# Kernel optimization log

Hardware: AMD Instinct MI355X
Metric: run time of the kernel (lower is better)

The kernel has to match this reference:

```python
import jax, jax.numpy as jnp
import numpy as np

NEG_INF = -1e9  # same masked_fill constant as the torch module
ALPHA = 0.1     # LeakyReLU negative slope


def setup_inputs() -> dict:
    key = jax.random.key(0)
    k1, k2, k3, k4, k5 = jax.random.split(key, 5)
    B, N, Din, Dout = 8, 2048, 512, 512
    features = jax.random.normal(k1, (B, N, Din), dtype=jnp.float32)
    graph = jax.random.randint(k2, (B, N, N), 0, 2, dtype=jnp.int64)
    # xavier_uniform with gain=1.414: limit = gain*sqrt(6/(fan_in+fan_out))
    lim_w = 1.414 * np.sqrt(6.0 / (Din + Dout))
    w = jax.random.uniform(k3, (Din, Dout), jnp.float32, -lim_w, lim_w)
    lim_a = 1.414 * np.sqrt(6.0 / (Dout + 1))
    a1 = jax.random.uniform(k4, (Dout, 1), jnp.float32, -lim_a, lim_a)
    a2 = jax.random.uniform(k5, (Dout, 1), jnp.float32, -lim_a, lim_a)
    return {"features": features, "graph": graph, "w": w, "a1": a1, "a2": a2}


def reference(features, graph, w, a1, a2):
    # hidden: [B, N, Dout]
    hidden = jnp.einsum("bni,io->bno", features, w)
    s1 = hidden @ a1  # [B, N, 1] -> broadcasts over columns
    s2 = hidden @ a2  # [B, N, 1] -> transposed broadcasts over rows
    # e[b,i,j] = leaky_relu(s1[b,i] + s2[b,j])
    e = jax.nn.leaky_relu(s1 + jnp.swapaxes(s2, 1, 2), negative_slope=ALPHA)
    e = jnp.where(graph == 0, NEG_INF, e)
    attn = jax.nn.softmax(e, axis=-1)  # [B, N, N]; dropout p=0 -> identity
    h_prime = jnp.einsum("bij,bjo->bio", attn, hidden)
    return jax.nn.elu(h_prime)  # concat=True
```

## Files before the change

kernel.cpp:

```cpp
#include <hip/hip_runtime.h>
#include <math.h>

#define B_ 8
#define N_ 2048
#define D_ 512
#define NROWS (B_ * N_)
#define HTS (NROWS + 32)
#define NEG_ALPHA 0.1f

typedef __bf16 bf16;
typedef __bf16 bf16x4 __attribute__((ext_vector_type(4)));
typedef __bf16 bf16x8 __attribute__((ext_vector_type(8)));
typedef float f32x4 __attribute__((ext_vector_type(4)));
typedef float f32x16 __attribute__((ext_vector_type(16)));

__global__ __launch_bounds__(256) void k_prep_wa(const float* __restrict__ W,
                                                 const float* __restrict__ a1,
                                                 const float* __restrict__ a2,
                                                 bf16* __restrict__ Wt,
                                                 float* __restrict__ wa1,
                                                 float* __restrict__ wa2) {
  const int t = threadIdx.x;
  const int bid = blockIdx.x;
#pragma unroll
  for (int p = 0; p < 2; ++p) {
    int din = t + p * 256;
    Wt[bid * D_ + din] = (bf16)W[(size_t)din * D_ + bid];
  }
  if (bid < 128) {
    const int wv = t >> 6, lane = t & 63;
    const int row = bid * 4 + wv;
    const float* wr = W + (size_t)row * D_;
    float d1 = 0.f, d2 = 0.f;
#pragma unroll
    for (int p = 0; p < 8; ++p) {
      int c = lane + p * 64;
      float w = wr[c];
      d1 = fmaf(w, a1[c], d1);
      d2 = fmaf(w, a2[c], d2);
    }
#pragma unroll
    for (int off = 32; off > 0; off >>= 1) {
      d1 += __shfl_down(d1, off, 64);
      d2 += __shfl_down(d2, off, 64);
    }
    if (lane == 0) {
      wa1[row] = d1;
      wa2[row] = d2;
    }
  }
}

__global__ __launch_bounds__(256) void k_scores_x(const float* __restrict__ X,
                                                  const float* __restrict__ wa1,
                                                  const float* __restrict__ wa2,
                                                  float* __restrict__ s1,
                                                  float* __restrict__ s2) {
  const int wv = threadIdx.x >> 6, lane = threadIdx.x & 63;
  const int r = blockIdx.x * 4 + wv;
  const float* x = X + (size_t)r * D_;
  float d1 = 0.f, d2 = 0.f;
#pragma unroll
  for (int p = 0; p < 2; ++p) {
    int c = lane * 4 + p * 256;
    float4 xv = *(const float4*)&x[c];
    float4 w1 = *(const float4*)&wa1[c];
    float4 w2 = *(const float4*)&wa2[c];
    d1 += xv.x * w1.x + xv.y * w1.y + xv.z * w1.z + xv.w * w1.w;
    d2 += xv.x * w2.x + xv.y * w2.y + xv.z * w2.z + xv.w * w2.w;
  }
#pragma unroll
  for (int off = 32; off > 0; off >>= 1) {
    d1 += __shfl_down(d1, off, 64);
    d2 += __shfl_down(d2, off, 64);
  }
  if (lane == 0) {
    s1[r] = d1;
    s2[r] = d2;
  }
}

#define LDH 40

__global__ __launch_bounds__(256, 2) void k_hiddenT(const float* __restrict__ X,
                                                    const bf16* __restrict__ Wt,
                                                    bf16* __restrict__ Ht) {
  __shared__ bf16 As[128][LDH];
  __shared__ bf16 Bs[128][LDH];
  const int t = threadIdx.x;
  const int m0 = blockIdx.y * 128;
  const int n0 = blockIdx.x * 128;
  const int lane = t & 63, w = t >> 6;
  const int wm = w >> 1, wn = w & 1;
  const int l15 = lane & 15, q = lane >> 4;

  f32x4 acc[4][4];
#pragma unroll
  for (int i = 0; i < 4; ++i)
#pragma unroll
    for (int j = 0; j < 4; ++j) acc[i][j] = (f32x4){0.f, 0.f, 0.f, 0.f};

  bf16x8 av[2];
  float4 bv[4];
#pragma unroll
  for (int p = 0; p < 2; ++p) {
    int s = t + p * 256;
    av[p] = *(const bf16x8*)&Wt[(size_t)(m0 + (s >> 2)) * D_ + (s & 3) * 8];
  }
#pragma unroll
  for (int p = 0; p < 4; ++p) {
    int s = t + p * 256;
    bv[p] = *(const float4*)&X[(size_t)(n0 + (s >> 3)) * D_ + (s & 7) * 4];
  }

  for (int k0 = 0; k0 < D_; k0 += 32) {
    __syncthreads();
#pragma unroll
    for (int p = 0; p < 2; ++p) {
      int s = t + p * 256;
      *(bf16x8*)&As[s >> 2][(s & 3) * 8] = av[p];
    }
#pragma unroll
    for (int p = 0; p < 4; ++p) {
      int s = t + p * 256;
      float4 v = bv[p];
      bf16x4 h = {(bf16)v.x, (bf16)v.y, (bf16)v.z, (bf16)v.w};
      *(bf16x4*)&Bs[s >> 3][(s & 7) * 4] = h;
    }
    __syncthreads();
    if (k0 + 32 < D_) {
#pragma unroll
      for (int p = 0; p < 2; ++p) {
        int s = t + p * 256;
        av[p] = *(const bf16x8*)&Wt[(size_t)(m0 + (s >> 2)) * D_ + k0 + 32 + (s & 3) * 8];
      }
#pragma unroll
      for (int p = 0; p < 4; ++p) {
        int s = t + p * 256;
        bv[p] = *(const float4*)&X[(size_t)(n0 + (s >> 3)) * D_ + k0 + 32 + (s & 7) * 4];
      }
    }
    bf16x8 a[4], bb[4];
#pragma unroll
    for (int i = 0; i < 4; ++i)
      a[i] = *(const bf16x8*)&As[wm * 64 + i * 16 + l15][q * 8];
#pragma unroll
    for (int j = 0; j < 4; ++j)
      bb[j] = *(const bf16x8*)&Bs[wn * 64 + j * 16 + l15][q * 8];
#pragma unroll
    for (int i = 0; i < 4; ++i)
#pragma unroll
      for (int j = 0; j < 4; ++j)
        acc[i][j] =
            __builtin_amdgcn_mfma_f32_16x16x32_bf16(a[i], bb[j], acc[i][j], 0, 0, 0);
  }
#pragma unroll
  for (int i = 0; i < 4; ++i)
#pragma unroll
    for (int r = 0; r < 4; ++r) {
      int dout = m0 + wm * 64 + i * 16 + q * 4 + r;
#pragma unroll
      for (int j = 0; j < 4; ++j) {
        int row = n0 + wn * 64 + j * 16 + l15;
        Ht[(size_t)dout * HTS + row] = (bf16)acc[i][j][r];
      }
    }
}

#define AT_BM 64
#define AT_BK 128
#define NCHUNK (N_ / AT_BK)
#define LDPS 136

__global__ __launch_bounds__(512, 1) void k_attn(const bf16* __restrict__ Ht,
                                                 const int* __restrict__ graph,
                                                 const float* __restrict__ s1,
                                                 const float* __restrict__ s2,
                                                 float* __restrict__ out) {
  __shared__ bf16 Ps[2][AT_BM][LDPS];
  __shared__ float s2s[N_];
  __shared__ float sum_part[AT_BM][8];
  __shared__ float row_sum[AT_BM];

  const int t = threadIdx.x;
  const int b = blockIdx.y;
  const int i0 = blockIdx.x * AT_BM;
  const int lane = t & 63, w = t >> 6;
  const int r31 = lane & 31, half = lane >> 5;
  const int d0 = w * 64;

  const bf16* Htb = Ht + (size_t)b * N_;
  const int* Gb = graph + ((size_t)b * N_ + i0) * N_;

  for (int c = t; c < N_; c += 512) s2s[c] = s2[b * N_ + c];

  const int pi = t >> 3;
  const int pj = (t & 7) * 16;
  const float s1r = s1[b * N_ + i0 + pi];
  float rsum = 0.f;

  f32x16 acc[2][2];
#pragma unroll
  for (int i = 0; i < 2; ++i)
#pragma unroll
    for (int j = 0; j < 2; ++j)
#pragma unroll
      for (int r = 0; r < 16; ++r) acc[i][j][r] = 0.f;

  int gg[16];
#pragma unroll
  for (int u = 0; u < 4; ++u)
    *(int4*)&gg[u * 4] = *(const int4*)&Gb[(size_t)pi * N_ + pj + u * 4];

  __syncthreads();

  float pv[16];
#pragma unroll
  for (int u = 0; u < 16; ++u) {
    float e = s1r + s2s[pj + u];
    e = (e > 0.f) ? e : NEG_ALPHA * e;
    float pe = (gg[u] != 0) ? __expf(e) : 0.f;
    pv[u] = pe;
    rsum += pe;
  }

  for (int p = 0; p < NCHUNK; ++p) {
    const int j0 = p * AT_BK;
    {
      bf16x8 w0 = {(bf16)pv[0], (bf16)pv[1], (bf16)pv[2], (bf16)pv[3],
                   (bf16)pv[4], (bf16)pv[5], (bf16)pv[6], (bf16)pv[7]};
      bf16x8 w1 = {(bf16)pv[8],  (bf16)pv[9],  (bf16)pv[10], (bf16)pv[11],
                   (bf16)pv[12], (bf16)pv[13], (bf16)pv[14], (bf16)pv[15]};
      *(bf16x8*)&Ps[p & 1][pi][pj] = w0;
      *(bf16x8*)&Ps[p & 1][pi][pj + 8] = w1;
    }
    if (p + 1 < NCHUNK) {
#pragma unroll
      for (int u = 0; u < 4; ++u)
        *(int4*)&gg[u * 4] =
            *(const int4*)&Gb[(size_t)pi * N_ + j0 + AT_BK + pj + u * 4];
    }
    __syncthreads();
#pragma unroll
    for (int ks = 0; ks < 8; ++ks) {
      const int ko = ks * 16 + half * 8;
      bf16x8 b0 = *(const bf16x8*)&Htb[(size_t)(d0 + r31) * HTS + j0 + ko];
      bf16x8 b1 = *(const bf16x8*)&Htb[(size_t)(d0 + 32 + r31) * HTS + j0 + ko];
      bf16x8 a0 = *(const bf16x8*)&Ps[p & 1][r31][ko];
      bf16x8 a1 = *(const bf16x8*)&Ps[p & 1][32 + r31][ko];
      acc[0][0] = __builtin_amdgcn_mfma_f32_32x32x16_bf16(a0, b0, acc[0][0], 0, 0, 0);
      acc[0][1] = __builtin_amdgcn_mfma_f32_32x32x16_bf16(a0, b1, acc[0][1], 0, 0, 0);
      acc[1][0] = __builtin_amdgcn_mfma_f32_32x32x16_bf16(a1, b0, acc[1][0], 0, 0, 0);
      acc[1][1] = __builtin_amdgcn_mfma_f32_32x32x16_bf16(a1, b1, acc[1][1], 0, 0, 0);
    }
    if (p + 1 < NCHUNK) {
#pragma unroll
      for (int u = 0; u < 16; ++u) {
        float e = s1r + s2s[j0 + AT_BK + pj + u];
        e = (e > 0.f) ? e : NEG_ALPHA * e;
        float pe = (gg[u] != 0) ? __expf(e) : 0.f;
        pv[u] = pe;
        rsum += pe;
      }
    }
  }

  sum_part[pi][t & 7] = rsum;
  __syncthreads();
  if (t < AT_BM) {
    float s = 0.f;
#pragma unroll
    for (int k = 0; k < 8; ++k) s += sum_part[t][k];
    row_sum[t] = s;
  }
  __syncthreads();

#pragma unroll
  for (int mt = 0; mt < 2; ++mt) {
    float inv[16];
#pragma unroll
    for (int r = 0; r < 16; ++r)
      inv[r] = 1.f / row_sum[mt * 32 + (r & 3) + 8 * (r >> 2) + 4 * half];
#pragma unroll
    for (int nt = 0; nt < 2; ++nt) {
      const int d = d0 + nt * 32 + r31;
#pragma unroll
      for (int r = 0; r < 16; ++r) {
        int i = mt * 32 + (r & 3) + 8 * (r >> 2) + 4 * half;
        float x = acc[mt][nt][r] * inv[r];
        out[((size_t)b * N_ + i0 + i) * D_ + d] = (x > 0.f) ? x : expm1f(x);
      }
    }
  }
}

extern "C" void kernel_launch(void* const* d_in, const int* in_sizes, int n_in,
                              void* d_out, int out_size, void* d_ws,
                              size_t ws_size, hipStream_t stream) {
  const float* X = (const float*)d_in[0];
  const int* graph = (const int*)d_in[1];
  const float* W = (const float*)d_in[2];
  const float* a1 = (const float*)d_in[3];
  const float* a2 = (const float*)d_in[4];
  float* out = (float*)d_out;

  char* ws = (char*)d_ws;
  bf16* Wt = (bf16*)ws;
  bf16* Ht = (bf16*)(ws + (1 << 19));
  float* s1 = (float*)(ws + (1 << 19) + (size_t)D_ * HTS * 2);
  float* s2 = s1 + NROWS;
  float* wa1 = s2 + NROWS;
  float* wa2 = wa1 + D_;

  hipLaunchKernelGGL(k_prep_wa, dim3(512), dim3(256), 0, stream, W, a1, a2, Wt,
                     wa1, wa2);
  hipLaunchKernelGGL(k_scores_x, dim3(NROWS / 4), dim3(256), 0, stream, X, wa1,
                     wa2, s1, s2);
  hipLaunchKernelGGL(k_hiddenT, dim3(NROWS / 128, D_ / 128), dim3(256), 0,
                     stream, X, Wt, Ht);
  hipLaunchKernelGGL(k_attn, dim3(N_ / AT_BM, B_), dim3(512), 0, stream, Ht,
                     graph, s1, s2, out);
}
```

Measured before the change: 324.7 us.

## Double-buffer hidden GEMM LDS and register-prefetch Ht tiles in attention kernel

```diff
diff --git a/kernel.cpp b/kernel.cpp
--- a/kernel.cpp
+++ b/kernel.cpp
@@ -85,8 +85,8 @@
 __global__ __launch_bounds__(256, 2) void k_hiddenT(const float* __restrict__ X,
                                                     const bf16* __restrict__ Wt,
                                                     bf16* __restrict__ Ht) {
-  __shared__ bf16 As[128][LDH];
-  __shared__ bf16 Bs[128][LDH];
+  __shared__ bf16 As[2][128][LDH];
+  __shared__ bf16 Bs[2][128][LDH];
   const int t = threadIdx.x;
   const int m0 = blockIdx.y * 128;
   const int n0 = blockIdx.x * 128;
@@ -113,19 +113,21 @@
     bv[p] = *(const float4*)&X[(size_t)(n0 + (s >> 3)) * D_ + (s & 7) * 4];
   }
 
-  for (int k0 = 0; k0 < D_; k0 += 32) {
-    __syncthreads();
+#pragma unroll
+  for (int it = 0; it < D_ / 32; ++it) {
+    const int k0 = it * 32;
+    const int buf = it & 1;
 #pragma unroll
     for (int p = 0; p < 2; ++p) {
       int s = t + p * 256;
-      *(bf16x8*)&As[s >> 2][(s & 3) * 8] = av[p];
+      *(bf16x8*)&As[buf][s >> 2][(s & 3) * 8] = av[p];
     }
 #pragma unroll
     for (int p = 0; p < 4; ++p) {
       int s = t + p * 256;
       float4 v = bv[p];
       bf16x4 h = {(bf16)v.x, (bf16)v.y, (bf16)v.z, (bf16)v.w};
-      *(bf16x4*)&Bs[s >> 3][(s & 7) * 4] = h;
+      *(bf16x4*)&Bs[buf][s >> 3][(s & 7) * 4] = h;
     }
     __syncthreads();
     if (k0 + 32 < D_) {
@@ -143,10 +145,10 @@
     bf16x8 a[4], bb[4];
 #pragma unroll
     for (int i = 0; i < 4; ++i)
-      a[i] = *(const bf16x8*)&As[wm * 64 + i * 16 + l15][q * 8];
+      a[i] = *(const bf16x8*)&As[buf][wm * 64 + i * 16 + l15][q * 8];
 #pragma unroll
     for (int j = 0; j < 4; ++j)
-      bb[j] = *(const bf16x8*)&Bs[wn * 64 + j * 16 + l15][q * 8];
+      bb[j] = *(const bf16x8*)&Bs[buf][wn * 64 + j * 16 + l15][q * 8];
 #pragma unroll
     for (int i = 0; i < 4; ++i)
 #pragma unroll
@@ -172,7 +174,7 @@
 #define NCHUNK (N_ / AT_BK)
 #define LDPS 136
 
-__global__ __launch_bounds__(512, 1) void k_attn(const bf16* __restrict__ Ht,
+__global__ __launch_bounds__(512, 2) void k_attn(const bf16* __restrict__ Ht,
                                                  const int* __restrict__ graph,
                                                  const float* __restrict__ s1,
                                                  const float* __restrict__ s2,
@@ -208,9 +210,17 @@
       for (int r = 0; r < 16; ++r) acc[i][j][r] = 0.f;
 
   int gg[16];
+  bf16x8 bp[2][16];
+
 #pragma unroll
   for (int u = 0; u < 4; ++u)
     *(int4*)&gg[u * 4] = *(const int4*)&Gb[(size_t)pi * N_ + pj + u * 4];
+#pragma unroll
+  for (int ks = 0; ks < 8; ++ks) {
+    const int ko = ks * 16 + half * 8;
+    bp[0][ks * 2 + 0] = *(const bf16x8*)&Htb[(size_t)(d0 + r31) * HTS + ko];
+    bp[0][ks * 2 + 1] = *(const bf16x8*)&Htb[(size_t)(d0 + 32 + r31) * HTS + ko];
+  }
 
   __syncthreads();
 
@@ -224,15 +234,17 @@
     rsum += pe;
   }
 
+#pragma unroll
   for (int p = 0; p < NCHUNK; ++p) {
     const int j0 = p * AT_BK;
+    const int cur = p & 1, nxt = cur ^ 1;
     {
       bf16x8 w0 = {(bf16)pv[0], (bf16)pv[1], (bf16)pv[2], (bf16)pv[3],
                    (bf16)pv[4], (bf16)pv[5], (bf16)pv[6], (bf16)pv[7]};
       bf16x8 w1 = {(bf16)pv[8],  (bf16)pv[9],  (bf16)pv[10], (bf16)pv[11],
                    (bf16)pv[12], (bf16)pv[13], (bf16)pv[14], (bf16)pv[15]};
-      *(bf16x8*)&Ps[p & 1][pi][pj] = w0;
-      *(bf16x8*)&Ps[p & 1][pi][pj + 8] = w1;
+      *(bf16x8*)&Ps[cur][pi][pj] = w0;
+      *(bf16x8*)&Ps[cur][pi][pj + 8] = w1;
     }
     if (p + 1 < NCHUNK) {
 #pragma unroll
@@ -241,13 +253,23 @@
             *(const int4*)&Gb[(size_t)pi * N_ + j0 + AT_BK + pj + u * 4];
     }
     __syncthreads();
+    if (p + 1 < NCHUNK) {
+#pragma unroll
+      for (int ks = 0; ks < 8; ++ks) {
+        const int ko = ks * 16 + half * 8;
+        bp[nxt][ks * 2 + 0] =
+            *(const bf16x8*)&Htb[(size_t)(d0 + r31) * HTS + j0 + AT_BK + ko];
+        bp[nxt][ks * 2 + 1] =
+            *(const bf16x8*)&Htb[(size_t)(d0 + 32 + r31) * HTS + j0 + AT_BK + ko];
+      }
+    }
 #pragma unroll
     for (int ks = 0; ks < 8; ++ks) {
       const int ko = ks * 16 + half * 8;
-      bf16x8 b0 = *(const bf16x8*)&Htb[(size_t)(d0 + r31) * HTS + j0 + ko];
-      bf16x8 b1 = *(const bf16x8*)&Htb[(size_t)(d0 + 32 + r31) * HTS + j0 + ko];
-      bf16x8 a0 = *(const bf16x8*)&Ps[p & 1][r31][ko];
-      bf16x8 a1 = *(const bf16x8*)&Ps[p & 1][32 + r31][ko];
+      bf16x8 a0 = *(const bf16x8*)&Ps[cur][r31][ko];
+      bf16x8 a1 = *(const bf16x8*)&Ps[cur][32 + r31][ko];
+      bf16x8 b0 = bp[cur][ks * 2 + 0];
+      bf16x8 b1 = bp[cur][ks * 2 + 1];
       acc[0][0] = __builtin_amdgcn_mfma_f32_32x32x16_bf16(a0, b0, acc[0][0], 0, 0, 0);
       acc[0][1] = __builtin_amdgcn_mfma_f32_32x32x16_bf16(a0, b1, acc[0][1], 0, 0, 0);
       acc[1][0] = __builtin_amdgcn_mfma_f32_32x32x16_bf16(a1, b0, acc[1][0], 0, 0, 0);
```

Measured after the change: 382.8 us. 17.9% more time.

## Stage GEMM and attention operands via async global-to-LDS copies with swizzled double buffers

Applied to the files above, without the earlier changes.

```diff
diff --git a/kernel.cpp b/kernel.cpp
--- a/kernel.cpp
+++ b/kernel.cpp
@@ -13,6 +13,12 @@
 typedef __bf16 bf16x8 __attribute__((ext_vector_type(8)));
 typedef float f32x4 __attribute__((ext_vector_type(4)));
 typedef float f32x16 __attribute__((ext_vector_type(16)));
+
+__device__ __forceinline__ void async_copy16(const void* g, void* l) {
+  __builtin_amdgcn_global_load_lds(
+      (const __attribute__((address_space(1))) void*)g,
+      (__attribute__((address_space(3))) void*)l, 16, 0, 0);
+}
 
 __global__ __launch_bounds__(256) void k_prep_wa(const float* __restrict__ W,
                                                  const float* __restrict__ a1,
@@ -51,12 +57,18 @@
   }
 }
 
-__global__ __launch_bounds__(256) void k_scores_x(const float* __restrict__ X,
-                                                  const float* __restrict__ wa1,
-                                                  const float* __restrict__ wa2,
-                                                  float* __restrict__ s1,
-                                                  float* __restrict__ s2) {
-  const int wv = threadIdx.x >> 6, lane = threadIdx.x & 63;
+__global__ __launch_bounds__(256) void k_conv_scores(
+    const float* __restrict__ X, const float* __restrict__ wa1,
+    const float* __restrict__ wa2, bf16* __restrict__ Xb,
+    float* __restrict__ s1, float* __restrict__ s2) {
+  __shared__ float was1[D_], was2[D_];
+  const int t = threadIdx.x;
+  for (int c = t; c < D_; c += 256) {
+    was1[c] = wa1[c];
+    was2[c] = wa2[c];
+  }
+  __syncthreads();
+  const int wv = t >> 6, lane = t & 63;
   const int r = blockIdx.x * 4 + wv;
   const float* x = X + (size_t)r * D_;
   float d1 = 0.f, d2 = 0.f;
@@ -64,10 +76,12 @@
   for (int p = 0; p < 2; ++p) {
     int c = lane * 4 + p * 256;
     float4 xv = *(const float4*)&x[c];
-    float4 w1 = *(const float4*)&wa1[c];
-    float4 w2 = *(const float4*)&wa2[c];
-    d1 += xv.x * w1.x + xv.y * w1.y + xv.z * w1.z + xv.w * w1.w;
-    d2 += xv.x * w2.x + xv.y * w2.y + xv.z * w2.z + xv.w * w2.w;
+    bf16x4 xb = {(bf16)xv.x, (bf16)xv.y, (bf16)xv.z, (bf16)xv.w};
+    *(bf16x4*)&Xb[(size_t)r * D_ + c] = xb;
+    d1 += xv.x * was1[c] + xv.y * was1[c + 1] + xv.z * was1[c + 2] +
+          xv.w * was1[c + 3];
+    d2 += xv.x * was2[c] + xv.y * was2[c + 1] + xv.z * was2[c + 2] +
+          xv.w * was2[c + 3];
   }
 #pragma unroll
   for (int off = 32; off > 0; off >>= 1) {
@@ -80,105 +94,105 @@
   }
 }
 
-#define LDH 40
-
-__global__ __launch_bounds__(256, 2) void k_hiddenT(const float* __restrict__ X,
+__global__ __launch_bounds__(256, 4) void k_hiddenT(const bf16* __restrict__ Xb,
                                                     const bf16* __restrict__ Wt,
                                                     bf16* __restrict__ Ht) {
-  __shared__ bf16 As[128][LDH];
-  __shared__ bf16 Bs[128][LDH];
+  __shared__ bf16 As[2][128 * 32];
+  __shared__ bf16 Bs[2][128 * 32];
   const int t = threadIdx.x;
   const int m0 = blockIdx.y * 128;
   const int n0 = blockIdx.x * 128;
   const int lane = t & 63, w = t >> 6;
   const int wm = w >> 1, wn = w & 1;
-  const int l15 = lane & 15, q = lane >> 4;
-
-  f32x4 acc[4][4];
-#pragma unroll
-  for (int i = 0; i < 4; ++i)
-#pragma unroll
-    for (int j = 0; j < 4; ++j) acc[i][j] = (f32x4){0.f, 0.f, 0.f, 0.f};
-
-  bf16x8 av[2];
-  float4 bv[4];
-#pragma unroll
-  for (int p = 0; p < 2; ++p) {
-    int s = t + p * 256;
-    av[p] = *(const bf16x8*)&Wt[(size_t)(m0 + (s >> 2)) * D_ + (s & 3) * 8];
-  }
-#pragma unroll
-  for (int p = 0; p < 4; ++p) {
-    int s = t + p * 256;
-    bv[p] = *(const float4*)&X[(size_t)(n0 + (s >> 3)) * D_ + (s & 7) * 4];
-  }
-
-  for (int k0 = 0; k0 < D_; k0 += 32) {
+  const int r31 = lane & 31, half = lane >> 5;
+
+  const char* WtB = (const char*)Wt;
+  const char* XbB = (const char*)Xb;
+
+  int srcA[2], srcB[2];
+#pragma unroll
+  for (int q = 0; q < 2; ++q) {
+    int g = (w * 2 + q) * 64 + lane;
+    int r = g >> 2, pc = g & 3;
+    int c = pc ^ (r & 3) ^ ((r >> 2) & 3);
+    srcA[q] = ((m0 + r) * D_ + c * 8) * 2;
+    srcB[q] = ((n0 + r) * D_ + c * 8) * 2;
+  }
+
+  f32x16 acc[2][2];
+#pragma unroll
+  for (int i = 0; i < 2; ++i)
+#pragma unroll
+    for (int j = 0; j < 2; ++j)
+#pragma unroll
+      for (int r = 0; r < 16; ++r) acc[i][j][r] = 0.f;
+
+#pragma unroll
+  for (int q = 0; q < 2; ++q) {
+    async_copy16(WtB + srcA[q], (char*)&As[0][0] + (w * 2 + q) * 1024);
+    async_copy16(XbB + srcB[q], (char*)&Bs[0][0] + (w * 2 + q) * 1024);
+  }
+
+#pragma unroll
+  for (int it = 0; it < D_ / 32; ++it) {
+    const int cur = it & 1;
     __syncthreads();
-#pragma unroll
-    for (int p = 0; p < 2; ++p) {
-      int s = t + p * 256;
-      *(bf16x8*)&As[s >> 2][(s & 3) * 8] = av[p];
-    }
-#pragma unroll
-    for (int p = 0; p < 4; ++p) {
-      int s = t + p * 256;
-      float4 v = bv[p];
-      bf16x4 h = {(bf16)v.x, (bf16)v.y, (bf16)v.z, (bf16)v.w};
-      *(bf16x4*)&Bs[s >> 3][(s & 7) * 4] = h;
-    }
-    __syncthreads();
-    if (k0 + 32 < D_) {
-#pragma unroll
-      for (int p = 0; p < 2; ++p) {
-        int s = t + p * 256;
-        av[p] = *(const bf16x8*)&Wt[(size_t)(m0 + (s >> 2)) * D_ + k0 + 32 + (s & 3) * 8];
+    if (it + 1 < D_ / 32) {
+      const int koff = (it + 1) * 64;
+#pragma unroll
+      for (int q = 0; q < 2; ++q) {
+        async_copy16(WtB + srcA[q] + koff,
+                     (char*)&As[cur ^ 1][0] + (w * 2 + q) * 1024);
+        async_copy16(XbB + srcB[q] + koff,
+                     (char*)&Bs[cur ^ 1][0] + (w * 2 + q) * 1024);
       }
-#pragma unroll
-      for (int p = 0; p < 4; ++p) {
-        int s = t + p * 256;
-        bv[p] = *(const float4*)&X[(size_t)(n0 + (s >> 3)) * D_ + k0 + 32 + (s & 7) * 4];
+    }
+#pragma unroll
+    for (int ks = 0; ks < 2; ++ks) {
+      const int ko = ks * 16 + half * 8;
+      const int c = ko >> 3;
+      int mA = wm * 64 + r31, mB = wm * 64 + 32 + r31;
+      int nA = wn * 64 + r31, nB = wn * 64 + 32 + r31;
+      int pmA = c ^ (mA & 3) ^ ((mA >> 2) & 3);
+      int pmB = c ^ (mB & 3) ^ ((mB >> 2) & 3);
+      int pnA = c ^ (nA & 3) ^ ((nA >> 2) & 3);
+      int pnB = c ^ (nB & 3) ^ ((nB >> 2) & 3);
+      bf16x8 a0 = *(const bf16x8*)((const char*)&As[cur][0] + mA * 64 + pmA * 16);
+      bf16x8 a1 = *(const bf16x8*)((const char*)&As[cur][0] + mB * 64 + pmB * 16);
+      bf16x8 b0 = *(const bf16x8*)((const char*)&Bs[cur][0] + nA * 64 + pnA * 16);
+      bf16x8 b1 = *(const bf16x8*)((const char*)&Bs[cur][0] + nB * 64 + pnB * 16);
+      acc[0][0] = __builtin_amdgcn_mfma_f32_32x32x16_bf16(a0, b0, acc[0][0], 0, 0, 0);
+      acc[0][1] = __builtin_amdgcn_mfma_f32_32x32x16_bf16(a0, b1, acc[0][1], 0, 0, 0);
+      acc[1][0] = __builtin_amdgcn_mfma_f32_32x32x16_bf16(a1, b0, acc[1][0], 0, 0, 0);
+      acc[1][1] = __builtin_amdgcn_mfma_f32_32x32x16_bf16(a1, b1, acc[1][1], 0, 0, 0);
+    }
+  }
+
+#pragma unroll
+  for (int mt = 0; mt < 2; ++mt)
+#pragma unroll
+    for (int r = 0; r < 16; ++r) {
+      int m = wm * 64 + mt * 32 + (r & 3) + 8 * (r >> 2) + 4 * half;
+#pragma unroll
+      for (int nt = 0; nt < 2; ++nt) {
+        int n = wn * 64 + nt * 32 + r31;
+        Ht[(size_t)(m0 + m) * HTS + n0 + n] = (bf16)acc[mt][nt][r];
       }
     }
-    bf16x8 a[4], bb[4];
-#pragma unroll
-    for (int i = 0; i < 4; ++i)
-      a[i] = *(const bf16x8*)&As[wm * 64 + i * 16 + l15][q * 8];
-#pragma unroll
-    for (int j = 0; j < 4; ++j)
-      bb[j] = *(const bf16x8*)&Bs[wn * 64 + j * 16 + l15][q * 8];
-#pragma unroll
-    for (int i = 0; i < 4; ++i)
-#pragma unroll
-      for (int j = 0; j < 4; ++j)
-        acc[i][j] =
-            __builtin_amdgcn_mfma_f32_16x16x32_bf16(a[i], bb[j], acc[i][j], 0, 0, 0);
-  }
-#pragma unroll
-  for (int i = 0; i < 4; ++i)
-#pragma unroll
-    for (int r = 0; r < 4; ++r) {
-      int dout = m0 + wm * 64 + i * 16 + q * 4 + r;
-#pragma unroll
-      for (int j = 0; j < 4; ++j) {
-        int row = n0 + wn * 64 + j * 16 + l15;
-        Ht[(size_t)dout * HTS + row] = (bf16)acc[i][j][r];
-      }
-    }
 }
 
 #define AT_BM 64
-#define AT_BK 128
-#define NCHUNK (N_ / AT_BK)
-#define LDPS 136
-
-__global__ __launch_bounds__(512, 1) void k_attn(const bf16* __restrict__ Ht,
+#define AT_BK 32
+#define NCH (N_ / AT_BK)
+#define PS_S 40
+
+__global__ __launch_bounds__(512, 4) void k_attn(const bf16* __restrict__ Ht,
                                                  const int* __restrict__ graph,
                                                  const float* __restrict__ s1,
                                                  const float* __restrict__ s2,
                                                  float* __restrict__ out) {
-  __shared__ bf16 Ps[2][AT_BM][LDPS];
-  __shared__ float s2s[N_];
+  __shared__ bf16 Hs[2][D_ * AT_BK];
+  __shared__ bf16 Ps[2][AT_BM][PS_S];
   __shared__ float sum_part[AT_BM][8];
   __shared__ float row_sum[AT_BM];
 
@@ -189,13 +203,12 @@
   const int r31 = lane & 31, half = lane >> 5;
   const int d0 = w * 64;
 
-  const bf16* Htb = Ht + (size_t)b * N_;
+  const char* HtB = (const char*)(Ht + (size_t)b * N_);
   const int* Gb = graph + ((size_t)b * N_ + i0) * N_;
-
-  for (int c = t; c < N_; c += 512) s2s[c] = s2[b * N_ + c];
+  const float* s2g = s2 + b * N_;
 
   const int pi = t >> 3;
-  const int pj = (t & 7) * 16;
+  const int pj = (t & 7) * 4;
   const float s1r = s1[b * N_ + i0 + pi];
   float rsum = 0.f;
 
@@ -207,60 +220,83 @@
 #pragma unroll
       for (int r = 0; r < 16; ++r) acc[i][j][r] = 0.f;
 
-  int gg[16];
-#pragma unroll
-  for (int u = 0; u < 4; ++u)
-    *(int4*)&gg[u * 4] = *(const int4*)&Gb[(size_t)pi * N_ + pj + u * 4];
-
-  __syncthreads();
-
-  float pv[16];
-#pragma unroll
-  for (int u = 0; u < 16; ++u) {
-    float e = s1r + s2s[pj + u];
-    e = (e > 0.f) ? e : NEG_ALPHA * e;
-    float pe = (gg[u] != 0) ? __expf(e) : 0.f;
-    pv[u] = pe;
-    rsum += pe;
-  }
-
-  for (int p = 0; p < NCHUNK; ++p) {
+  int dsrc[4];
+#pragma unroll
+  for (int q = 0; q < 4; ++q) {
+    int g = (w * 4 + q) * 64 + lane;
+    int d = g >> 2, pc = g & 3;
+    int c = pc ^ (d & 3) ^ ((d >> 2) & 3);
+    dsrc[q] = d * (HTS * 2) + c * 16;
+  }
+
+  int4 gg[2];
+  float4 sv[2];
+  gg[0] = *(const int4*)&Gb[(size_t)pi * N_ + pj];
+  sv[0] = *(const float4*)&s2g[pj];
+  gg[1] = *(const int4*)&Gb[(size_t)pi * N_ + 32 + pj];
+  sv[1] = *(const float4*)&s2g[32 + pj];
+#pragma unroll
+  for (int q = 0; q < 4; ++q)
+    async_copy16(HtB + dsrc[q], (char*)&Hs[0][0] + (w * 4 + q) * 1024);
+
+  float pv[4];
+  {
+    int gA[4] = {gg[0].x, gg[0].y, gg[0].z, gg[0].w};
+    float sA[4] = {sv[0].x, sv[0].y, sv[0].z, sv[0].w};
+#pragma unroll
+    for (int u = 0; u < 4; ++u) {
+      float e = s1r + sA[u];
+      e = (e > 0.f) ? e : NEG_ALPHA * e;
+      pv[u] = (gA[u] != 0) ? __expf(e) : 0.f;
+      rsum += pv[u];
+    }
+  }
+
+#pragma unroll 2
+  for (int p = 0; p < NCH; ++p) {
+    const int cur = p & 1;
     const int j0 = p * AT_BK;
     {
-      bf16x8 w0 = {(bf16)pv[0], (bf16)pv[1], (bf16)pv[2], (bf16)pv[3],
-                   (bf16)pv[4], (bf16)pv[5], (bf16)pv[6], (bf16)pv[7]};
-      bf16x8 w1 = {(bf16)pv[8],  (bf16)pv[9],  (bf16)pv[10], (bf16)pv[11],
-                   (bf16)pv[12], (bf16)pv[13], (bf16)pv[14], (bf16)pv[15]};
-      *(bf16x8*)&Ps[p & 1][pi][pj] = w0;
-      *(bf16x8*)&Ps[p & 1][pi][pj + 8] = w1;
-    }
-    if (p + 1 < NCHUNK) {
-#pragma unroll
-      for (int u = 0; u < 4; ++u)
-        *(int4*)&gg[u * 4] =
-            *(const int4*)&Gb[(size_t)pi * N_ + j0 + AT_BK + pj + u * 4];
+      bf16x4 pb = {(bf16)pv[0], (bf16)pv[1], (bf16)pv[2], (bf16)pv[3]};
+      *(bf16x4*)&Ps[cur][pi][pj] = pb;
     }
     __syncthreads();
-#pragma unroll
-    for (int ks = 0; ks < 8; ++ks) {
+    if (p + 2 < NCH) {
+      gg[cur] = *(const int4*)&Gb[(size_t)pi * N_ + j0 + 64 + pj];
+      sv[cur] = *(const float4*)&s2g[j0 + 64 + pj];
+    }
+    if (p + 1 < NCH) {
+#pragma unroll
+      for (int q = 0; q < 4; ++q)
+        async_copy16(HtB + dsrc[q] + (j0 + AT_BK) * 2,
+                     (char*)&Hs[cur ^ 1][0] + (w * 4 + q) * 1024);
+    }
+#pragma unroll
+    for (int ks = 0; ks < 2; ++ks) {
       const int ko = ks * 16 + half * 8;
-      bf16x8 b0 = *(const bf16x8*)&Htb[(size_t)(d0 + r31) * HTS + j0 + ko];
-      bf16x8 b1 = *(const bf16x8*)&Htb[(size_t)(d0 + 32 + r31) * HTS + j0 + ko];
-      bf16x8 a0 = *(const bf16x8*)&Ps[p & 1][r31][ko];
-      bf16x8 a1 = *(const bf16x8*)&Ps[p & 1][32 + r31][ko];
+      const int c = ko >> 3;
+      int dA = d0 + r31, dB = d0 + 32 + r31;
+      int pA = c ^ (dA & 3) ^ ((dA >> 2) & 3);
+      int pB = c ^ (dB & 3) ^ ((dB >> 2) & 3);
+      bf16x8 a0 = *(const bf16x8*)&Ps[cur][r31][ko];
+      bf16x8 a1 = *(const bf16x8*)&Ps[cur][32 + r31][ko];
+      bf16x8 b0 = *(const bf16x8*)((const char*)&Hs[cur][0] + dA * 64 + pA * 16);
+      bf16x8 b1 = *(const bf16x8*)((const char*)&Hs[cur][0] + dB * 64 + pB * 16);
       acc[0][0] = __builtin_amdgcn_mfma_f32_32x32x16_bf16(a0, b0, acc[0][0], 0, 0, 0);
       acc[0][1] = __builtin_amdgcn_mfma_f32_32x32x16_bf16(a0, b1, acc[0][1], 0, 0, 0);
       acc[1][0] = __builtin_amdgcn_mfma_f32_32x32x16_bf16(a1, b0, acc[1][0], 0, 0, 0);
       acc[1][1] = __builtin_amdgcn_mfma_f32_32x32x16_bf16(a1, b1, acc[1][1], 0, 0, 0);
     }
-    if (p + 1 < NCHUNK) {
-#pragma unroll
-      for (int u = 0; u < 16; ++u) {
-        float e = s1r + s2s[j0 + AT_BK + pj + u];
+    if (p + 1 < NCH) {
+      const int nx = cur ^ 1;
+      int gA[4] = {gg[nx].x, gg[nx].y, gg[nx].z, gg[nx].w};
+      float sA[4] = {sv[nx].x, sv[nx].y, sv[nx].z, sv[nx].w};
+#pragma unroll
+      for (int u = 0; u < 4; ++u) {
+        float e = s1r + sA[u];
         e = (e > 0.f) ? e : NEG_ALPHA * e;
-        float pe = (gg[u] != 0) ? __expf(e) : 0.f;
-        pv[u] = pe;
-        rsum += pe;
+        pv[u] = (gA[u] != 0) ? __expf(e) : 0.f;
+        rsum += pv[u];
       }
     }
   }
@@ -307,17 +343,18 @@
   char* ws = (char*)d_ws;
   bf16* Wt = (bf16*)ws;
   bf16* Ht = (bf16*)(ws + (1 << 19));
-  float* s1 = (float*)(ws + (1 << 19) + (size_t)D_ * HTS * 2);
-  float* s2 = s1 + NROWS;
-  float* wa1 = s2 + NROWS;
-  float* wa2 = wa1 + D_;
+  bf16* Xb = (bf16*)(ws + 17334272);
+  float* s1 = (float*)(ws + 34111488);
+  float* s2 = (float*)(ws + 34177024);
+  float* wa1 = (float*)(ws + 34242560);
+  float* wa2 = (float*)(ws + 34244608);
 
   hipLaunchKernelGGL(k_prep_wa, dim3(512), dim3(256), 0, stream, W, a1, a2, Wt,
                      wa1, wa2);
-  hipLaunchKernelGGL(k_scores_x, dim3(NROWS / 4), dim3(256), 0, stream, X, wa1,
-                     wa2, s1, s2);
+  hipLaunchKernelGGL(k_conv_scores, dim3(NROWS / 4), dim3(256), 0, stream, X,
+                     wa1, wa2, Xb, s1, s2);
   hipLaunchKernelGGL(k_hiddenT, dim3(NROWS / 128, D_ / 128), dim3(256), 0,
-                     stream, X, Wt, Ht);
+                     stream, Xb, Wt, Ht);
   hipLaunchKernelGGL(k_attn, dim3(N_ / AT_BM, B_), dim3(512), 0, stream, Ht,
                      graph, s1, s2, out);
 }
```

Result: slower. 366.4 us (+12.8%).
